# Kernel optimization log

Hardware: AMD Instinct MI355X
Metric: run time of the kernel (lower is better)

The kernel has to match this reference:

```python
import jax, jax.numpy as jnp
import numpy as np
import math

B, S, DIM = 2, 2048, 2048
NH = 16
HD = DIM // NH  # 128
RANK = 32


def setup_inputs() -> dict:
    key = jax.random.key(0)
    ks = jax.random.split(key, 10)
    x = jax.random.normal(ks[0], (B, S, DIM), dtype=jnp.float32)
    # causal additive mask (use -1e9 instead of -inf for grad-safety)
    mask = jnp.where(jnp.tril(jnp.ones((S, S), dtype=bool)), 0.0, -1e9).astype(jnp.float32)[None, None]
    # rotary frequencies, as in llama: theta = 10000^{-2i/d}
    inv_freq = 1.0 / (10000.0 ** (jnp.arange(0, HD, 2, dtype=jnp.float32) / HD))  # [HD/2]
    t = jnp.arange(S, dtype=jnp.float32)
    freqs = jnp.outer(t, inv_freq)  # [S, HD/2]
    freqs_cos = jnp.cos(freqs)
    freqs_sin = jnp.sin(freqs)
    scale = 0.02
    wq = jax.random.normal(ks[1], (DIM, DIM), dtype=jnp.float32) * scale
    wk = jax.random.normal(ks[2], (DIM, DIM), dtype=jnp.float32) * scale
    wv = jax.random.normal(ks[3], (DIM, DIM), dtype=jnp.float32) * scale
    wo = jax.random.normal(ks[4], (DIM, DIM), dtype=jnp.float32) * scale
    wa_q = jax.random.normal(ks[5], (RANK, DIM), dtype=jnp.float32) * 0.02
    wa_k = jax.random.normal(ks[6], (RANK, DIM), dtype=jnp.float32) * 0.02
    return {"x": x, "mask": mask, "freqs_cos": freqs_cos, "freqs_sin": freqs_sin,
            "wq": wq, "wk": wk, "wv": wv, "wo": wo, "wa_q": wa_q, "wa_k": wa_k}


def _apply_rope(t, cos, sin):
    # t: [B, S, H, HD]; cos/sin: [S, HD/2]
    tr = t.reshape(*t.shape[:-1], HD // 2, 2)
    tre, tim = tr[..., 0], tr[..., 1]
    c = cos[None, :, None, :]
    s = sin[None, :, None, :]
    out_re = tre * c - tim * s
    out_im = tre * s + tim * c
    return jnp.stack([out_re, out_im], axis=-1).reshape(t.shape)


def reference(x, mask, freqs_cos, freqs_sin, wq, wk, wv, wo, wa_q, wa_k):
    bsz, seqlen, dim = x.shape
    xq = (x @ wq.T).reshape(bsz, seqlen, NH, HD)
    xk = (x @ wk.T).reshape(bsz, seqlen, NH, HD)
    xv = (x @ wv.T).reshape(bsz, seqlen, NH, HD)
    # low-rank adaptive gate (computed on detached x in the original)
    xd = jax.lax.stop_gradient(x)
    xq_h = xd @ wa_q.T  # [B, S, 32]
    xk_h = xd @ wa_k.T  # [B, S, 32]
    adaptive_mask = jnp.einsum('bqr,bkr->bqk', xq_h, xk_h)  # [B, S, S]

    xq = _apply_rope(xq, freqs_cos, freqs_sin)
    xk = _apply_rope(xk, freqs_cos, freqs_sin)

    q = xq.transpose(0, 2, 1, 3)  # [B, H, S, HD]
    k = xk.transpose(0, 2, 1, 3)
    v = xv.transpose(0, 2, 1, 3)

    scores = jnp.einsum('bhqd,bhkd->bhqk', q, k) / math.sqrt(HD)
    scores = scores + mask
    scores = jax.nn.softmax(scores.astype(jnp.float32), axis=-1).astype(q.dtype)
    scores = scores * jax.nn.sigmoid(adaptive_mask)[:, None]  # gate, broadcast over heads
    out = jnp.einsum('bhqk,bhkd->bhqd', scores, v)
    out = out.transpose(0, 2, 1, 3).reshape(bsz, seqlen, -1)
    return out @ wo.T
```

## Files before the change

kernel.cpp:

```cpp
#include <hip/hip_runtime.h>

typedef __attribute__((ext_vector_type(8))) short short8v;
typedef __attribute__((ext_vector_type(4))) short short4v;
typedef __attribute__((ext_vector_type(4))) float floatx4;

#define S_    2048
#define DIM_  2048

#define ASG(p) ((__attribute__((address_space(1))) void*)(p))
#define ASL(p) ((__attribute__((address_space(3))) void*)(p))

__device__ __forceinline__ short f2bf(float f){
  union { float f; unsigned u; } c; c.f = f;
  unsigned u = c.u;
  unsigned r = (u + 0x7fffu + ((u >> 16) & 1u)) >> 16;
  return (short)r;
}
__device__ __forceinline__ float bf2f(short s){
  union { unsigned u; float f; } c; c.u = ((unsigned)(unsigned short)s) << 16;
  return c.f;
}

__global__ __launch_bounds__(256) void cvt_k(const float* __restrict__ in,
                                             short* __restrict__ out, int n){
  int i = blockIdx.x*256 + threadIdx.x;
  int idx = i*4;
  if (idx >= n) return;
  floatx4 v = *(const floatx4*)(in + idx);
  short4v o;
  o[0]=f2bf(v[0]); o[1]=f2bf(v[1]); o[2]=f2bf(v[2]); o[3]=f2bf(v[3]);
  *(short4v*)(out + idx) = o;
}

template<bool OUT_BF16>
__global__ __launch_bounds__(256,2)
void gemm_nt_fast(const short* __restrict__ A, const short* __restrict__ B,
                  void* __restrict__ Cout, int M, int N, int K){
  __shared__ short As[128][64];
  __shared__ short Bs[128][64];
  int tid = threadIdx.x;
  int wave = tid>>6, lane = tid&63, quad = lane>>4, l16 = lane&15;
  int l7 = l16&7;
  int m0 = blockIdx.x*128, n0 = blockIdx.y*128;
  int wm = (wave>>1)*64, wn = (wave&1)*64;
  floatx4 acc[4][4] = {};

  int lr = lane>>3;
  int sw = (lane&7) ^ lr;
  const short* Abase = A + (size_t)(m0 + wave*32 + lr)*K + sw*8;
  const short* Bbase = B + (size_t)(n0 + wave*32 + lr)*K + sw*8;

  for (int k0 = 0; k0 < K; k0 += 64){
    __syncthreads();
    #pragma unroll
    for (int i=0;i<4;i++){
      __builtin_amdgcn_global_load_lds(ASG(Abase + (size_t)(i*8)*K + k0),
                                       ASL(&As[wave*32 + i*8][0]), 16, 0, 0);
      __builtin_amdgcn_global_load_lds(ASG(Bbase + (size_t)(i*8)*K + k0),
                                       ASL(&Bs[wave*32 + i*8][0]), 16, 0, 0);
    }
    __syncthreads();
    #pragma unroll
    for (int ks=0; ks<2; ks++){
      short8v af[4], bf[4];
      #pragma unroll
      for (int i=0;i<4;i++) af[i] = *(short8v*)&As[wm + i*16 + l16][((ks*4+quad)^l7)*8];
      #pragma unroll
      for (int j=0;j<4;j++) bf[j] = *(short8v*)&Bs[wn + j*16 + l16][((ks*4+quad)^l7)*8];
      #pragma unroll
      for (int i=0;i<4;i++)
        #pragma unroll
        for (int j=0;j<4;j++)
          acc[i][j] = __builtin_amdgcn_mfma_f32_16x16x32_bf16(af[i], bf[j], acc[i][j], 0,0,0);
    }
  }
  #pragma unroll
  for (int i=0;i<4;i++){
    #pragma unroll
    for (int r=0;r<4;r++){
      int gm = m0 + wm + i*16 + quad*4 + r;
      #pragma unroll
      for (int j=0;j<4;j++){
        int gn = n0 + wn + j*16 + l16;
        if (OUT_BF16) ((short*)Cout)[(size_t)gm*N + gn] = f2bf(acc[i][j][r]);
        else          ((float*)Cout)[(size_t)gm*N + gn] = acc[i][j][r];
      }
    }
  }
}

__global__ __launch_bounds__(256) void rope_k(short* __restrict__ Q, short* __restrict__ Kv,
                                              const float* __restrict__ fcos,
                                              const float* __restrict__ fsin){
  int i = blockIdx.x*256 + threadIdx.x;
  int row = i >> 10;
  int p = i & 1023;
  int s = row & (S_-1);
  int pp = p & 63;
  float c = fcos[s*64+pp], sn = fsin[s*64+pp];
  {
    size_t a = (size_t)row*2176 + p*2;
    int v = *(int*)(Q + a);
    float re = bf2f((short)(v & 0xffff)), im = bf2f((short)(v >> 16));
    float orr = re*c - im*sn, oi = re*sn + im*c;
    *(int*)(Q + a) = ((int)(unsigned short)f2bf(oi) << 16) | (unsigned short)f2bf(orr);
  }
  {
    size_t a = (size_t)row*2048 + p*2;
    int v = *(int*)(Kv + a);
    float re = bf2f((short)(v & 0xffff)), im = bf2f((short)(v >> 16));
    float orr = re*c - im*sn, oi = re*sn + im*c;
    *(int*)(Kv + a) = ((int)(unsigned short)f2bf(oi) << 16) | (unsigned short)f2bf(orr);
  }
}

__global__ __launch_bounds__(256) void transpose_k(const short* __restrict__ V,
                                                   short* __restrict__ Vt){
  __shared__ short t[64][72];
  int b = blockIdx.z;
  int s0 = blockIdx.x*64, n0 = blockIdx.y*64;
  int tid = threadIdx.x;
  #pragma unroll
  for (int i=0;i<2;i++){
    int c = tid + 256*i;
    int r = c>>3, cc = (c&7)*8;
    *(short8v*)&t[r][cc] = *(const short8v*)&V[((size_t)(b*2048 + s0 + r))*2048 + n0 + cc];
  }
  __syncthreads();
  #pragma unroll
  for (int i=0;i<2;i++){
    int c = tid + 256*i;
    int r = c>>3, cc = (c&7)*8;
    short8v v;
    #pragma unroll
    for (int u=0;u<8;u++) v[u] = t[cc+u][r];
    *(short8v*)&Vt[((size_t)(b*2048 + n0 + r))*2048 + s0 + cc] = v;
  }
}

__global__ __launch_bounds__(256,2)
void flash_k(const short* __restrict__ Qc, const short* __restrict__ Kk,
             const short* __restrict__ Vt, short* __restrict__ O){
  int pi = blockIdx.x, h = blockIdx.y, b = blockIdx.z;
  int tid = threadIdx.x, wave = tid>>6, lane = tid&63, quad = lane>>4, l16 = lane&15;
  int l7 = l16&7;

  __shared__ short Ks [64][128];
  __shared__ short Vts[128][64];
  __shared__ short KHs[64][40];
  __shared__ short Ps [4][16][72];

  const float CS = 1.44269504f * 0.08838834764831845f;
  const float NL2E = -1.44269504f;

  for (int ph = 0; ph < 2; ph++){
    int qt = ph ? pi : 31 - pi;
    size_t qrow = (size_t)(b*2048 + qt*64 + wave*16 + l16);
    short8v qf[4];
    #pragma unroll
    for (int ks=0;ks<4;ks++)
      qf[ks] = *(const short8v*)&Qc[qrow*2176 + h*128 + ks*32 + quad*8];
    short8v qh = *(const short8v*)&Qc[qrow*2176 + 2048 + quad*8];

    floatx4 oacc[8] = {};
    float lp[4] = {0.f,0.f,0.f,0.f};

    for (int kt=0; kt<=qt; kt++){
      int k0 = kt*64;
      __syncthreads();
      {
        const short* Ksrc = Kk + ((size_t)(b*2048 + k0 + wave*16))*2048 + h*128;
        int r4 = lane>>4, c16 = lane&15;
        #pragma unroll
        for (int j=0;j<4;j++)
          __builtin_amdgcn_global_load_lds(
            ASG(Ksrc + (size_t)(j*4 + r4)*2048 + ((c16 ^ r4 ^ ((j&1)*4))*8)),
            ASL(&Ks[wave*16 + j*4][0]), 16, 0, 0);
        const short* Vsrc = Vt + ((size_t)(b*2048 + h*128 + wave*32 + (lane>>3)))*2048 + k0
                            + (((lane&7) ^ (lane>>3))*8);
        #pragma unroll
        for (int j=0;j<4;j++)
          __builtin_amdgcn_global_load_lds(
            ASG(Vsrc + (size_t)(j*8)*2048),
            ASL(&Vts[wave*32 + j*8][0]), 16, 0, 0);
        int r = tid>>2, c = tid&3;
        short8v kh = *(const short8v*)&Qc[(size_t)(b*2048 + k0 + r)*2176 + 2080 + c*8];
        *(short8v*)&KHs[r][c*8] = kh;
      }
      __syncthreads();

      floatx4 sacc[4] = {};
      #pragma unroll
      for (int j=0;j<4;j++)
        #pragma unroll
        for (int ks2=0;ks2<4;ks2++){
          short8v kf = *(short8v*)&Ks[j*16+l16][((ks2*4+quad)^l7)*8];
          sacc[j] = __builtin_amdgcn_mfma_f32_16x16x32_bf16(qf[ks2], kf, sacc[j], 0,0,0);
        }
      floatx4 am[4];
      #pragma unroll
      for (int j=0;j<4;j++){
        short8v khf = *(short8v*)&KHs[j*16+l16][quad*8];
        floatx4 z = {0.f,0.f,0.f,0.f};
        am[j] = __builtin_amdgcn_mfma_f32_16x16x32_bf16(qh, khf, z, 0,0,0);
      }
      bool diag = (kt == qt);
      int qin = wave*16 + quad*4;
      #pragma unroll
      for (int j=0;j<4;j++){
        int kin = j*16 + l16;
        #pragma unroll
        for (int r=0;r<4;r++){
          bool keep = !diag || (kin <= qin + r);
          float p = keep ? __builtin_amdgcn_exp2f(sacc[j][r]*CS) : 0.f;
          float g = __builtin_amdgcn_rcpf(1.f + __builtin_amdgcn_exp2f(am[j][r]*NL2E));
          lp[r] += p;
          Ps[wave][quad*4+r][j*16+l16] = f2bf(p*g);
        }
      }
      #pragma unroll
      for (int ks2=0; ks2<2; ks2++){
        short8v pf = *(short8v*)&Ps[wave][l16][ks2*32 + quad*8];
        #pragma unroll
        for (int dt=0; dt<8; dt++){
          short8v vf = *(short8v*)&Vts[dt*16 + l16][((ks2*4+quad)^l7)*8];
          oacc[dt] = __builtin_amdgcn_mfma_f32_16x16x32_bf16(pf, vf, oacc[dt], 0,0,0);
        }
      }
    }

    #pragma unroll
    for (int r=0;r<4;r++)
      #pragma unroll
      for (int off=1; off<16; off<<=1)
        lp[r] += __shfl_xor(lp[r], off, 64);
    #pragma unroll
    for (int r=0;r<4;r++){
      float inv = __builtin_amdgcn_rcpf(lp[r]);
      size_t orow = (size_t)(b*2048 + qt*64 + wave*16 + quad*4 + r);
      #pragma unroll
      for (int dt=0;dt<8;dt++)
        O[orow*2048 + h*128 + dt*16 + l16] = f2bf(oacc[dt][r]*inv);
    }
  }
}

extern "C" void kernel_launch(void* const* d_in, const int* in_sizes, int n_in,
                              void* d_out, int out_size, void* d_ws, size_t ws_size,
                              hipStream_t stream){
  const float* x    = (const float*)d_in[0];
  const float* fcos = (const float*)d_in[2];
  const float* fsin = (const float*)d_in[3];
  const float* wq   = (const float*)d_in[4];
  const float* wk   = (const float*)d_in[5];
  const float* wv   = (const float*)d_in[6];
  const float* wo   = (const float*)d_in[7];
  const float* waq  = (const float*)d_in[8];
  const float* wak  = (const float*)d_in[9];
  float* out = (float*)d_out;

  char* ws = (char*)d_ws;
  size_t off = 0;
  const size_t SZ_ACT = (size_t)4096*2048*2;
  const size_t SZ_W   = (size_t)2048*2048*2;
  short* xb   = (short*)(ws + off); off += SZ_ACT;
  short* Wcat = (short*)(ws + off); off += (size_t)2176*2048*2;
  short* wkb  = (short*)(ws + off); off += SZ_W;
  short* wvb  = (short*)(ws + off); off += SZ_W;
  short* wob  = (short*)(ws + off); off += SZ_W;
  short* Qcat = (short*)(ws + off); off += (size_t)4096*2176*2;
  short* Kb   = (short*)(ws + off); off += SZ_ACT;
  short* Vb   = (short*)(ws + off); off += SZ_ACT;
  short* Vtb  = (short*)(ws + off); off += SZ_ACT;
  short* Ob   = xb;

  cvt_k<<<8192,256,0,stream>>>(x,   xb,  8388608);
  cvt_k<<<4096,256,0,stream>>>(wq,  Wcat, 4194304);
  cvt_k<<<64,  256,0,stream>>>(waq, Wcat + 4194304, 65536);
  cvt_k<<<64,  256,0,stream>>>(wak, Wcat + 4259840, 65536);
  cvt_k<<<4096,256,0,stream>>>(wk,  wkb, 4194304);
  cvt_k<<<4096,256,0,stream>>>(wv,  wvb, 4194304);
  cvt_k<<<4096,256,0,stream>>>(wo,  wob, 4194304);

  gemm_nt_fast<true><<<dim3(32,17),256,0,stream>>>(xb, Wcat, Qcat, 4096, 2176, 2048);
  gemm_nt_fast<true><<<dim3(32,16),256,0,stream>>>(xb, wkb, Kb, 4096, 2048, 2048);
  gemm_nt_fast<true><<<dim3(32,16),256,0,stream>>>(xb, wvb, Vb, 4096, 2048, 2048);

  rope_k<<<16384,256,0,stream>>>(Qcat, Kb, fcos, fsin);
  transpose_k<<<dim3(32,32,2),256,0,stream>>>(Vb, Vtb);

  flash_k<<<dim3(16,16,2),256,0,stream>>>(Qcat, Kb, Vtb, Ob);

  gemm_nt_fast<false><<<dim3(32,16),256,0,stream>>>(Ob, wob, out, 4096, 2048, 2048);
}
```

Measured before the change: 448.0 us.

## Fuse QKV GEMMs, transpose V in epilogue, precompute gate, double-buffer flash

Weight conversions are merged into one kernel, and Q, gate-projection, K and V are computed by a single fused GEMM over a concatenated weight matrix. V's transpose is written from that GEMM's epilogue through LDS, which removes the separate transpose kernel. The sigmoid gate is precomputed into a tiled buffer by a new kernel and read by flash attention. Q's RoPE moves into the flash kernel's Q load, and the flash kernel double-buffers its K/V LDS tiles so the next tile's load overlaps compute. The trade-off is extra global traffic for the gate buffer and larger LDS use, which could reduce occupancy.

```diff
diff --git a/kernel.cpp b/kernel.cpp
--- a/kernel.cpp
+++ b/kernel.cpp
@@ -6,6 +6,7 @@
 
 #define S_    2048
 #define DIM_  2048
+#define NW_   6272
 
 #define ASG(p) ((__attribute__((address_space(1))) void*)(p))
 #define ASL(p) ((__attribute__((address_space(3))) void*)(p))
@@ -32,10 +33,121 @@
   *(short4v*)(out + idx) = o;
 }
 
-template<bool OUT_BF16>
+__global__ __launch_bounds__(256)
+void cvt_w(const float* wq, const float* waq, const float* wak,
+           const float* wk, const float* wv, const float* wo,
+           short* Wcat, short* wob){
+  const float* src; short* dst; int n;
+  switch (blockIdx.y){
+    case 0: src=wq;  dst=Wcat;                 n=4194304; break;
+    case 1: src=waq; dst=Wcat+(size_t)2048*2048; n=65536; break;
+    case 2: src=wak; dst=Wcat+(size_t)2080*2048; n=65536; break;
+    case 3: src=wk;  dst=Wcat+(size_t)2112*2048; n=4194304; break;
+    case 4: src=wv;  dst=Wcat+(size_t)4224*2048; n=4194304; break;
+    case 5: src=wo;  dst=wob;                  n=4194304; break;
+    default: {
+      int idx = (blockIdx.x*256 + threadIdx.x)*4;
+      if (idx < 131072){
+        short4v z = {0,0,0,0};
+        *(short4v*)(Wcat + (size_t)4160*2048 + idx) = z;
+      }
+      return;
+    }
+  }
+  int idx = (blockIdx.x*256 + threadIdx.x)*4;
+  if (idx >= n) return;
+  floatx4 v = *(const floatx4*)(src + idx);
+  short4v o;
+  o[0]=f2bf(v[0]); o[1]=f2bf(v[1]); o[2]=f2bf(v[2]); o[3]=f2bf(v[3]);
+  *(short4v*)(dst + idx) = o;
+}
+
+__global__ __launch_bounds__(256,4)
+void gemm_qkv(const short* __restrict__ A, const short* __restrict__ B,
+              short* __restrict__ Cout, short* __restrict__ Vt){
+  __shared__ short SH[2][128][64];
+  short (*As)[64] = SH[0];
+  short (*Bs)[64] = SH[1];
+  const int K = 2048, N = NW_;
+  int tid = threadIdx.x;
+  int wave = tid>>6, lane = tid&63, quad = lane>>4, l16 = lane&15;
+  int l7 = l16&7;
+  int m0 = blockIdx.x*128, n0 = blockIdx.y*128;
+  int wm = (wave>>1)*64, wn = (wave&1)*64;
+  floatx4 acc[4][4] = {};
+
+  int lr = lane>>3;
+  int sw = (lane&7) ^ lr;
+  const short* Abase = A + (size_t)(m0 + wave*32 + lr)*K + sw*8;
+  const short* Bbase = B + (size_t)(n0 + wave*32 + lr)*K + sw*8;
+
+  for (int k0 = 0; k0 < K; k0 += 64){
+    __syncthreads();
+    #pragma unroll
+    for (int i=0;i<4;i++){
+      __builtin_amdgcn_global_load_lds(ASG(Abase + (size_t)(i*8)*K + k0),
+                                       ASL(&As[wave*32 + i*8][0]), 16, 0, 0);
+      __builtin_amdgcn_global_load_lds(ASG(Bbase + (size_t)(i*8)*K + k0),
+                                       ASL(&Bs[wave*32 + i*8][0]), 16, 0, 0);
+    }
+    __syncthreads();
+    #pragma unroll
+    for (int ks=0; ks<2; ks++){
+      short8v af[4], bf[4];
+      #pragma unroll
+      for (int i=0;i<4;i++) af[i] = *(short8v*)&As[wm + i*16 + l16][((ks*4+quad)^l7)*8];
+      #pragma unroll
+      for (int j=0;j<4;j++) bf[j] = *(short8v*)&Bs[wn + j*16 + l16][((ks*4+quad)^l7)*8];
+      #pragma unroll
+      for (int i=0;i<4;i++)
+        #pragma unroll
+        for (int j=0;j<4;j++)
+          acc[i][j] = __builtin_amdgcn_mfma_f32_16x16x32_bf16(af[i], bf[j], acc[i][j], 0,0,0);
+    }
+  }
+
+  if (n0 < 4224){
+    #pragma unroll
+    for (int i=0;i<4;i++)
+      #pragma unroll
+      for (int r=0;r<4;r++){
+        int gm = m0 + wm + i*16 + quad*4 + r;
+        #pragma unroll
+        for (int j=0;j<4;j++){
+          int gn = n0 + wn + j*16 + l16;
+          Cout[(size_t)gm*N + gn] = f2bf(acc[i][j][r]);
+        }
+      }
+  } else {
+    short* T = &SH[0][0][0];
+    __syncthreads();
+    #pragma unroll
+    for (int i=0;i<4;i++){
+      int mb = wm + i*16 + quad*4;
+      int mc = mb>>3, mi = mb&7;
+      #pragma unroll
+      for (int j=0;j<4;j++){
+        int n = wn + j*16 + l16;
+        short4v p;
+        p[0]=f2bf(acc[i][j][0]); p[1]=f2bf(acc[i][j][1]);
+        p[2]=f2bf(acc[i][j][2]); p[3]=f2bf(acc[i][j][3]);
+        *(short4v*)&T[n*128 + ((mc ^ (n&7))*8) + mi] = p;
+      }
+    }
+    __syncthreads();
+    int nl = tid>>1, half = tid&1;
+    #pragma unroll
+    for (int c=0;c<8;c++){
+      int cc = half*8 + c;
+      short8v v = *(short8v*)&T[nl*128 + ((cc ^ (nl&7))*8)];
+      *(short8v*)&Vt[(size_t)(n0 - 4224 + nl)*4096 + m0 + cc*8] = v;
+    }
+  }
+}
+
 __global__ __launch_bounds__(256,2)
-void gemm_nt_fast(const short* __restrict__ A, const short* __restrict__ B,
-                  void* __restrict__ Cout, int M, int N, int K){
+void gemm_nt_f32(const short* __restrict__ A, const short* __restrict__ B,
+                 float* __restrict__ Cout, int M, int N, int K){
   __shared__ short As[128][64];
   __shared__ short Bs[128][64];
   int tid = threadIdx.x;
@@ -75,21 +187,19 @@
     }
   }
   #pragma unroll
-  for (int i=0;i<4;i++){
+  for (int i=0;i<4;i++)
     #pragma unroll
     for (int r=0;r<4;r++){
       int gm = m0 + wm + i*16 + quad*4 + r;
       #pragma unroll
       for (int j=0;j<4;j++){
         int gn = n0 + wn + j*16 + l16;
-        if (OUT_BF16) ((short*)Cout)[(size_t)gm*N + gn] = f2bf(acc[i][j][r]);
-        else          ((float*)Cout)[(size_t)gm*N + gn] = acc[i][j][r];
-      }
-    }
-  }
-}
-
-__global__ __launch_bounds__(256) void rope_k(short* __restrict__ Q, short* __restrict__ Kv,
+        Cout[(size_t)gm*N + gn] = acc[i][j][r];
+      }
+    }
+}
+
+__global__ __launch_bounds__(256) void rope_k(short* __restrict__ X,
                                               const float* __restrict__ fcos,
                                               const float* __restrict__ fsin){
   int i = blockIdx.x*256 + threadIdx.x;
@@ -98,112 +208,116 @@
   int s = row & (S_-1);
   int pp = p & 63;
   float c = fcos[s*64+pp], sn = fsin[s*64+pp];
-  {
-    size_t a = (size_t)row*2176 + p*2;
-    int v = *(int*)(Q + a);
-    float re = bf2f((short)(v & 0xffff)), im = bf2f((short)(v >> 16));
-    float orr = re*c - im*sn, oi = re*sn + im*c;
-    *(int*)(Q + a) = ((int)(unsigned short)f2bf(oi) << 16) | (unsigned short)f2bf(orr);
-  }
-  {
-    size_t a = (size_t)row*2048 + p*2;
-    int v = *(int*)(Kv + a);
-    float re = bf2f((short)(v & 0xffff)), im = bf2f((short)(v >> 16));
-    float orr = re*c - im*sn, oi = re*sn + im*c;
-    *(int*)(Kv + a) = ((int)(unsigned short)f2bf(oi) << 16) | (unsigned short)f2bf(orr);
-  }
-}
-
-__global__ __launch_bounds__(256) void transpose_k(const short* __restrict__ V,
-                                                   short* __restrict__ Vt){
-  __shared__ short t[64][72];
-  int b = blockIdx.z;
-  int s0 = blockIdx.x*64, n0 = blockIdx.y*64;
-  int tid = threadIdx.x;
+  size_t a = (size_t)row*NW_ + 2112 + p*2;
+  int v = *(int*)(X + a);
+  float re = bf2f((short)(v & 0xffff)), im = bf2f((short)(v >> 16));
+  float orr = re*c - im*sn, oi = re*sn + im*c;
+  *(int*)(X + a) = ((int)(unsigned short)f2bf(oi) << 16) | (unsigned short)f2bf(orr);
+}
+
+__global__ __launch_bounds__(256)
+void gate_k(const short* __restrict__ X, short* __restrict__ G){
+  int kt = blockIdx.x, qt = blockIdx.y, b = blockIdx.z;
+  if (kt > qt) return;
+  int tid = threadIdx.x, wave = tid>>6, lane = tid&63, quad = lane>>4, l16 = lane&15;
+  const float NL2E = -1.44269504f;
+
+  short8v qh = *(const short8v*)&X[(size_t)(b*2048 + qt*64 + wave*16 + l16)*NW_ + 2048 + quad*8];
+  floatx4 am[4];
   #pragma unroll
-  for (int i=0;i<2;i++){
-    int c = tid + 256*i;
-    int r = c>>3, cc = (c&7)*8;
-    *(short8v*)&t[r][cc] = *(const short8v*)&V[((size_t)(b*2048 + s0 + r))*2048 + n0 + cc];
-  }
-  __syncthreads();
+  for (int j=0;j<4;j++){
+    short8v kh = *(const short8v*)&X[(size_t)(b*2048 + kt*64 + j*16 + l16)*NW_ + 2080 + quad*8];
+    floatx4 z = {0.f,0.f,0.f,0.f};
+    am[j] = __builtin_amdgcn_mfma_f32_16x16x32_bf16(qh, kh, z, 0,0,0);
+  }
+  short* Gd = G + (((size_t)(b*32 + kt)*2048) + qt*64 + wave*16 + quad*4)*64 + l16*4;
   #pragma unroll
-  for (int i=0;i<2;i++){
-    int c = tid + 256*i;
-    int r = c>>3, cc = (c&7)*8;
-    short8v v;
-    #pragma unroll
-    for (int u=0;u<8;u++) v[u] = t[cc+u][r];
-    *(short8v*)&Vt[((size_t)(b*2048 + n0 + r))*2048 + s0 + cc] = v;
+  for (int r=0;r<4;r++){
+    short4v sv;
+    #pragma unroll
+    for (int j=0;j<4;j++){
+      float g = __builtin_amdgcn_rcpf(1.f + __builtin_amdgcn_exp2f(am[j][r]*NL2E));
+      sv[j] = f2bf(g);
+    }
+    *(short4v*)(Gd + (size_t)r*64) = sv;
   }
 }
 
 __global__ __launch_bounds__(256,2)
-void flash_k(const short* __restrict__ Qc, const short* __restrict__ Kk,
-             const short* __restrict__ Vt, short* __restrict__ O){
+void flash_k(const short* __restrict__ Qc, const short* __restrict__ Vt,
+             const short* __restrict__ G, const float* __restrict__ fcos,
+             const float* __restrict__ fsin, short* __restrict__ O){
   int pi = blockIdx.x, h = blockIdx.y, b = blockIdx.z;
   int tid = threadIdx.x, wave = tid>>6, lane = tid&63, quad = lane>>4, l16 = lane&15;
   int l7 = l16&7;
 
-  __shared__ short Ks [64][128];
-  __shared__ short Vts[128][64];
-  __shared__ short KHs[64][40];
+  __shared__ short Ks [2][64][128];
+  __shared__ short Vts[2][128][64];
   __shared__ short Ps [4][16][72];
 
   const float CS = 1.44269504f * 0.08838834764831845f;
-  const float NL2E = -1.44269504f;
+
+  auto stage = [&](int kt, int buf){
+    int k0 = kt*64;
+    const short* Ksrc = Qc + ((size_t)(b*2048 + k0 + wave*16))*NW_ + 2112 + h*128;
+    int r4 = lane>>4, c16 = lane&15;
+    #pragma unroll
+    for (int j=0;j<4;j++)
+      __builtin_amdgcn_global_load_lds(
+        ASG(Ksrc + (size_t)(j*4 + r4)*NW_ + ((c16 ^ r4 ^ ((j&1)*4))*8)),
+        ASL(&Ks[buf][wave*16 + j*4][0]), 16, 0, 0);
+    const short* Vsrc = Vt + ((size_t)(h*128 + wave*32 + (lane>>3)))*4096 + b*2048 + k0
+                        + (((lane&7) ^ (lane>>3))*8);
+    #pragma unroll
+    for (int j=0;j<4;j++)
+      __builtin_amdgcn_global_load_lds(
+        ASG(Vsrc + (size_t)(j*8)*4096),
+        ASL(&Vts[buf][wave*32 + j*8][0]), 16, 0, 0);
+  };
 
   for (int ph = 0; ph < 2; ph++){
     int qt = ph ? pi : 31 - pi;
     size_t qrow = (size_t)(b*2048 + qt*64 + wave*16 + l16);
+    int srow = qt*64 + wave*16 + l16;
     short8v qf[4];
     #pragma unroll
     for (int ks=0;ks<4;ks++)
-      qf[ks] = *(const short8v*)&Qc[qrow*2176 + h*128 + ks*32 + quad*8];
-    short8v qh = *(const short8v*)&Qc[qrow*2176 + 2048 + quad*8];
+      qf[ks] = *(const short8v*)&Qc[qrow*NW_ + h*128 + ks*32 + quad*8];
+    #pragma unroll
+    for (int ks=0;ks<4;ks++)
+      #pragma unroll
+      for (int jj=0;jj<4;jj++){
+        float re = bf2f(qf[ks][2*jj]), im = bf2f(qf[ks][2*jj+1]);
+        int p = ks*16 + quad*4 + jj;
+        float c = fcos[srow*64 + p], sn = fsin[srow*64 + p];
+        qf[ks][2*jj]   = f2bf(re*c - im*sn);
+        qf[ks][2*jj+1] = f2bf(re*sn + im*c);
+      }
 
     floatx4 oacc[8] = {};
     float lp[4] = {0.f,0.f,0.f,0.f};
 
+    __syncthreads();
+    stage(0, 0);
     for (int kt=0; kt<=qt; kt++){
-      int k0 = kt*64;
       __syncthreads();
-      {
-        const short* Ksrc = Kk + ((size_t)(b*2048 + k0 + wave*16))*2048 + h*128;
-        int r4 = lane>>4, c16 = lane&15;
-        #pragma unroll
-        for (int j=0;j<4;j++)
-          __builtin_amdgcn_global_load_lds(
-            ASG(Ksrc + (size_t)(j*4 + r4)*2048 + ((c16 ^ r4 ^ ((j&1)*4))*8)),
-            ASL(&Ks[wave*16 + j*4][0]), 16, 0, 0);
-        const short* Vsrc = Vt + ((size_t)(b*2048 + h*128 + wave*32 + (lane>>3)))*2048 + k0
-                            + (((lane&7) ^ (lane>>3))*8);
-        #pragma unroll
-        for (int j=0;j<4;j++)
-          __builtin_amdgcn_global_load_lds(
-            ASG(Vsrc + (size_t)(j*8)*2048),
-            ASL(&Vts[wave*32 + j*8][0]), 16, 0, 0);
-        int r = tid>>2, c = tid&3;
-        short8v kh = *(const short8v*)&Qc[(size_t)(b*2048 + k0 + r)*2176 + 2080 + c*8];
-        *(short8v*)&KHs[r][c*8] = kh;
-      }
-      __syncthreads();
+      if (kt < qt) stage(kt+1, (kt+1)&1);
+      int bc = kt&1;
+
+      const short* gb = G + (((size_t)(b*32 + kt)*2048) + qt*64 + wave*16 + quad*4)*64 + l16*4;
+      short4v g4[4];
+      #pragma unroll
+      for (int r=0;r<4;r++) g4[r] = *(const short4v*)(gb + (size_t)r*64);
 
       floatx4 sacc[4] = {};
       #pragma unroll
       for (int j=0;j<4;j++)
         #pragma unroll
         for (int ks2=0;ks2<4;ks2++){
-          short8v kf = *(short8v*)&Ks[j*16+l16][((ks2*4+quad)^l7)*8];
+          short8v kf = *(short8v*)&Ks[bc][j*16+l16][((ks2*4+quad)^l7)*8];
           sacc[j] = __builtin_amdgcn_mfma_f32_16x16x32_bf16(qf[ks2], kf, sacc[j], 0,0,0);
         }
-      floatx4 am[4];
-      #pragma unroll
-      for (int j=0;j<4;j++){
-        short8v khf = *(short8v*)&KHs[j*16+l16][quad*8];
-        floatx4 z = {0.f,0.f,0.f,0.f};
-        am[j] = __builtin_amdgcn_mfma_f32_16x16x32_bf16(qh, khf, z, 0,0,0);
-      }
+
       bool diag = (kt == qt);
       int qin = wave*16 + quad*4;
       #pragma unroll
@@ -213,9 +327,8 @@
         for (int r=0;r<4;r++){
           bool keep = !diag || (kin <= qin + r);
           float p = keep ? __builtin_amdgcn_exp2f(sacc[j][r]*CS) : 0.f;
-          float g = __builtin_amdgcn_rcpf(1.f + __builtin_amdgcn_exp2f(am[j][r]*NL2E));
           lp[r] += p;
-          Ps[wave][quad*4+r][j*16+l16] = f2bf(p*g);
+          Ps[wave][quad*4+r][j*16+l16] = f2bf(p * bf2f(g4[r][j]));
         }
       }
       #pragma unroll
@@ -223,7 +336,7 @@
         short8v pf = *(short8v*)&Ps[wave][l16][ks2*32 + quad*8];
         #pragma unroll
         for (int dt=0; dt<8; dt++){
-          short8v vf = *(short8v*)&Vts[dt*16 + l16][((ks2*4+quad)^l7)*8];
+          short8v vf = *(short8v*)&Vts[bc][dt*16 + l16][((ks2*4+quad)^l7)*8];
           oacc[dt] = __builtin_amdgcn_mfma_f32_16x16x32_bf16(pf, vf, oacc[dt], 0,0,0);
         }
       }
@@ -261,35 +374,23 @@
 
   char* ws = (char*)d_ws;
   size_t off = 0;
-  const size_t SZ_ACT = (size_t)4096*2048*2;
-  const size_t SZ_W   = (size_t)2048*2048*2;
-  short* xb   = (short*)(ws + off); off += SZ_ACT;
-  short* Wcat = (short*)(ws + off); off += (size_t)2176*2048*2;
-  short* wkb  = (short*)(ws + off); off += SZ_W;
-  short* wvb  = (short*)(ws + off); off += SZ_W;
-  short* wob  = (short*)(ws + off); off += SZ_W;
-  short* Qcat = (short*)(ws + off); off += (size_t)4096*2176*2;
-  short* Kb   = (short*)(ws + off); off += SZ_ACT;
-  short* Vb   = (short*)(ws + off); off += SZ_ACT;
-  short* Vtb  = (short*)(ws + off); off += SZ_ACT;
-  short* Ob   = xb;
-
-  cvt_k<<<8192,256,0,stream>>>(x,   xb,  8388608);
-  cvt_k<<<4096,256,0,stream>>>(wq,  Wcat, 4194304);
-  cvt_k<<<64,  256,0,stream>>>(waq, Wcat + 4194304, 65536);
-  cvt_k<<<64,  256,0,stream>>>(wak, Wcat + 4259840, 65536);
-  cvt_k<<<4096,256,0,stream>>>(wk,  wkb, 4194304);
-  cvt_k<<<4096,256,0,stream>>>(wv,  wvb, 4194304);
-  cvt_k<<<4096,256,0,stream>>>(wo,  wob, 4194304);
-
-  gemm_nt_fast<true><<<dim3(32,17),256,0,stream>>>(xb, Wcat, Qcat, 4096, 2176, 2048);
-  gemm_nt_fast<true><<<dim3(32,16),256,0,stream>>>(xb, wkb, Kb, 4096, 2048, 2048);
-  gemm_nt_fast<true><<<dim3(32,16),256,0,stream>>>(xb, wvb, Vb, 4096, 2048, 2048);
-
-  rope_k<<<16384,256,0,stream>>>(Qcat, Kb, fcos, fsin);
-  transpose_k<<<dim3(32,32,2),256,0,stream>>>(Vb, Vtb);
-
-  flash_k<<<dim3(16,16,2),256,0,stream>>>(Qcat, Kb, Vtb, Ob);
-
-  gemm_nt_fast<false><<<dim3(32,16),256,0,stream>>>(Ob, wob, out, 4096, 2048, 2048);
-}
+  short* xb   = (short*)(ws + off); off += (size_t)4096*2048*2;
+  short* Wcat = (short*)(ws + off); off += (size_t)NW_*2048*2;
+  short* wob  = (short*)(ws + off); off += (size_t)2048*2048*2;
+  short* XQKV = (short*)(ws + off); off += (size_t)4096*NW_*2;
+  short* Vtb  = (short*)(ws + off); off += (size_t)2048*4096*2;
+  short* G    = xb;
+  short* Ob   = Wcat;
+
+  cvt_k<<<8192,256,0,stream>>>(x, xb, 8388608);
+  cvt_w<<<dim3(4096,7),256,0,stream>>>(wq, waq, wak, wk, wv, wo, Wcat, wob);
+
+  gemm_qkv<<<dim3(32,49),256,0,stream>>>(xb, Wcat, XQKV, Vtb);
+
+  rope_k<<<16384,256,0,stream>>>(XQKV, fcos, fsin);
+  gate_k<<<dim3(32,32,2),256,0,stream>>>(XQKV, G);
+
+  flash_k<<<dim3(16,16,2),256,0,stream>>>(XQKV, Vtb, G, fcos, fsin, Ob);
+
+  gemm_nt_f32<<<dim3(32,16),256,0,stream>>>(Ob, wob, out, 4096, 2048, 2048);
+}
```

New measurement: 422.6 us. -5.7%, faster.
